# Optimization experiments

Measured on AMD Instinct MI355X. Metric: run time of the kernel, lower is better.

Reference implementation:

```python
import jax, jax.numpy as jnp
import numpy as np

N, E, F_IN, H, G, A, OUT = 50000, 800000, 128, 256, 64, 8, 1


def _lin(k, fi, fo):
    s = 1.0 / np.sqrt(fi)
    kw, kb = jax.random.split(k)
    W = jax.random.uniform(kw, (fi, fo), jnp.float32, -s, s)
    b = jax.random.uniform(kb, (fo,), jnp.float32, -s, s)
    return W, b


def setup_inputs() -> dict:
    key = jax.random.key(0)
    ks = jax.random.split(key, 12)
    x = jax.random.normal(ks[0], (N, F_IN), jnp.float32)
    edge_index = jax.random.randint(ks[1], (2, E), 0, N, dtype=jnp.int64)
    batch = jnp.sort(jax.random.randint(ks[2], (N,), 0, G, dtype=jnp.int64))
    graph_attr = jax.random.normal(ks[3], (G, A), jnp.float32)
    W1, b1 = _lin(ks[4], F_IN, H)
    W2, b2 = _lin(ks[5], H, H)
    W3, b3 = _lin(ks[6], H, H)
    fcW1, fcb1 = _lin(ks[7], H + A, H)
    fcW2, fcb2 = _lin(ks[8], H, OUT)
    ones = jnp.ones((H,), jnp.float32)
    zeros = jnp.zeros((H,), jnp.float32)
    return dict(x=x, graph_attr=graph_attr, edge_index=edge_index, batch=batch,
                W1=W1, b1=b1, W2=W2, b2=b2, W3=W3, b3=b3,
                g1=ones, be1=zeros, g2=ones, be2=zeros, g3=ones, be3=zeros,
                fcW1=fcW1, fcb1=fcb1, fcW2=fcW2, fcb2=fcb2)


def gcn_conv(x, W, b, src, dst, n):
    # PyG GCNConv: add self-loops, symmetric normalization, xW then scatter-add
    xw = x @ W  # [N, H]
    loop = jnp.arange(n)
    src2 = jnp.concatenate([src, loop])
    dst2 = jnp.concatenate([dst, loop])
    deg = jnp.zeros((n,), xw.dtype).at[dst2].add(1.0)
    dinv = jnp.where(deg > 0, jax.lax.rsqrt(deg), 0.0)
    norm = dinv[src2] * dinv[dst2]  # [E+N]
    out = jnp.zeros((n, xw.shape[1]), xw.dtype).at[dst2].add(xw[src2] * norm[:, None])
    return out + b


def layer_norm(x, g, b, eps=1e-5):
    m = x.mean(-1, keepdims=True)
    v = ((x - m) ** 2).mean(-1, keepdims=True)
    return (x - m) * jax.lax.rsqrt(v + eps) * g + b


def reference(x, graph_attr, edge_index, batch,
              W1, b1, W2, b2, W3, b3,
              g1, be1, g2, be2, g3, be3,
              fcW1, fcb1, fcW2, fcb2):
    src, dst = edge_index[0], edge_index[1]
    h = jax.nn.relu(layer_norm(gcn_conv(x, W1, b1, src, dst, N), g1, be1))
    h = jax.nn.relu(layer_norm(gcn_conv(h, W2, b2, src, dst, N), g2, be2))
    h = jax.nn.relu(layer_norm(gcn_conv(h, W3, b3, src, dst, N), g3, be3))
    # global mean pool over graph ids
    sums = jax.ops.segment_sum(h, batch, num_segments=G)
    cnts = jax.ops.segment_sum(jnp.ones((N,), h.dtype), batch, num_segments=G)
    pooled = sums / jnp.maximum(cnts, 1.0)[:, None]  # [G, H]
    z = jnp.concatenate([pooled, graph_attr.reshape(-1, A)], axis=1)
    z = jax.nn.relu(z @ fcW1 + fcb1)
    return z @ fcW2 + fcb2  # [G, OUT]
```

## Files before the change

### kernel.cpp

```cpp
#include <hip/hip_runtime.h>
#include <hip/hip_bf16.h>

#define N_NODES 50000
#define N_EDGES 800000
#define F_IN    128
#define H_DIM   256
#define G_NUM   64
#define A_DIM   8

#define NBUCKET 196
#define NCHUNK  391
#define CHUNK   2048
#define K4CAP   6144

typedef __attribute__((ext_vector_type(8))) short short8v;
typedef __attribute__((ext_vector_type(4))) float float4v;
typedef __attribute__((ext_vector_type(2))) float float2v;

__device__ __forceinline__ float b2f(unsigned short u) {
    return __uint_as_float(((unsigned int)u) << 16);
}
__device__ __forceinline__ unsigned short f2b(float v) {
    return __hip_bfloat16_raw(__float2bfloat16(v)).x;
}
__device__ __forceinline__ unsigned char f2fp8(float v) {
    return (unsigned char)(__builtin_amdgcn_cvt_pk_fp8_f32(v, v, 0, false) & 0xff);
}
__device__ __forceinline__ unsigned int pack2(float a, float b) {
    return (unsigned int)f2b(a) | ((unsigned int)f2b(b) << 16);
}
__device__ __forceinline__ void accadd16(float2v* a, uint4 v) {
    a[0] += __builtin_amdgcn_cvt_pk_f32_fp8((int)v.x, false);
    a[1] += __builtin_amdgcn_cvt_pk_f32_fp8((int)v.x, true);
    a[2] += __builtin_amdgcn_cvt_pk_f32_fp8((int)v.y, false);
    a[3] += __builtin_amdgcn_cvt_pk_f32_fp8((int)v.y, true);
    a[4] += __builtin_amdgcn_cvt_pk_f32_fp8((int)v.z, false);
    a[5] += __builtin_amdgcn_cvt_pk_f32_fp8((int)v.z, true);
    a[6] += __builtin_amdgcn_cvt_pk_f32_fp8((int)v.w, false);
    a[7] += __builtin_amdgcn_cvt_pk_f32_fp8((int)v.w, true);
}
__device__ __forceinline__ void accfma16(float2v* a, uint4 v, float w) {
    float2v w2 = {w, w};
    a[0] = __builtin_amdgcn_cvt_pk_f32_fp8((int)v.x, false) * w2 + a[0];
    a[1] = __builtin_amdgcn_cvt_pk_f32_fp8((int)v.x, true)  * w2 + a[1];
    a[2] = __builtin_amdgcn_cvt_pk_f32_fp8((int)v.y, false) * w2 + a[2];
    a[3] = __builtin_amdgcn_cvt_pk_f32_fp8((int)v.y, true)  * w2 + a[3];
    a[4] = __builtin_amdgcn_cvt_pk_f32_fp8((int)v.z, false) * w2 + a[4];
    a[5] = __builtin_amdgcn_cvt_pk_f32_fp8((int)v.z, true)  * w2 + a[5];
    a[6] = __builtin_amdgcn_cvt_pk_f32_fp8((int)v.w, false) * w2 + a[6];
    a[7] = __builtin_amdgcn_cvt_pk_f32_fp8((int)v.w, true)  * w2 + a[7];
}

#define SK 40


__global__ __launch_bounds__(512) void fuse0_kernel(const int* __restrict__ dst,
                                                    unsigned int* __restrict__ Hg,
                                                    const float* __restrict__ x,
                                                    const float* __restrict__ W1,
                                                    unsigned char* __restrict__ P8,
                                                    const float* __restrict__ W2,
                                                    unsigned short* __restrict__ Wt2,
                                                    const float* __restrict__ W3,
                                                    unsigned short* __restrict__ Wt3) {
    const int CB = NCHUNK;
    const int GB = (N_NODES + 127) / 128;
    int b = blockIdx.x, t = threadIdx.x;
    if (b < CB) {
        __shared__ unsigned int h[256];
        if (t < 256) h[t] = 0u;
        __syncthreads();
        int base = b * CHUNK;
        #pragma unroll
        for (int k = 0; k < 4; k++) {
            int i = base + k * 512 + t;
            if (i < N_EDGES) atomicAdd(&h[dst[i] >> 8], 1u);
        }
        __syncthreads();
        if (t < 256) Hg[(size_t)t * NCHUNK + b] = h[t];
        return;
    }
    b -= CB;
    if (b < GB) {
        __shared__ unsigned short As[128][SK];
        __shared__ unsigned short Bs[256][SK];
        int wave = t >> 6, lane = t & 63;
        int wm0 = (wave & 1) * 64, wn0 = (wave >> 1) * 64;
        int bm = b * 128;
        int l15 = lane & 15, lq = lane >> 4;
        float4v acc[4][4];
        #pragma unroll
        for (int i = 0; i < 4; i++)
            #pragma unroll
            for (int j = 0; j < 4; j++)
                acc[i][j] = (float4v){0.f, 0.f, 0.f, 0.f};

        for (int k0 = 0; k0 < F_IN; k0 += 32) {
            {
                int row = t >> 2, koff = (t & 3) * 8;
                short8v tmp = (short8v){0,0,0,0,0,0,0,0};
                if (bm + row < N_NODES) {
                    const float* xp = x + (size_t)(bm + row) * F_IN + k0 + koff;
                    float4 a0 = *(const float4*)xp;
                    float4 a1 = *(const float4*)(xp + 4);
                    tmp[0] = (short)f2b(a0.x); tmp[1] = (short)f2b(a0.y);
                    tmp[2] = (short)f2b(a0.z); tmp[3] = (short)f2b(a0.w);
                    tmp[4] = (short)f2b(a1.x); tmp[5] = (short)f2b(a1.y);
                    tmp[6] = (short)f2b(a1.z); tmp[7] = (short)f2b(a1.w);
                }
                *(short8v*)&As[row][koff] = tmp;
            }
            #pragma unroll
            for (int h = 0; h < 2; h++) {
                int c = t + h * 512;
                int n = c >> 2, koff = (c & 3) * 8;
                short8v tmp;
                #pragma unroll
                for (int kk = 0; kk < 8; kk++)
                    tmp[kk] = (short)f2b(W1[(size_t)(k0 + koff + kk) * H_DIM + n]);
                *(short8v*)&Bs[n][koff] = tmp;
            }
            __syncthreads();
            short8v af[4], bf[4];
            #pragma unroll
            for (int i = 0; i < 4; i++) {
                af[i] = *(const short8v*)&As[wm0 + i * 16 + l15][lq * 8];
                bf[i] = *(const short8v*)&Bs[wn0 + i * 16 + l15][lq * 8];
            }
            #pragma unroll
            for (int i = 0; i < 4; i++)
                #pragma unroll
                for (int j = 0; j < 4; j++)
                    acc[i][j] = __builtin_amdgcn_mfma_f32_16x16x32_bf16(af[i], bf[j], acc[i][j], 0, 0, 0);
            __syncthreads();
        }
        #pragma unroll
        for (int i = 0; i < 4; i++) {
            #pragma unroll
            for (int r = 0; r < 4; r++) {
                int row = bm + wm0 + i * 16 + lq * 4 + r;
                if (row < N_NODES) {
                    #pragma unroll
                    for (int j = 0; j < 4; j++) {
                        int col = wn0 + j * 16 + l15;
                        P8[(size_t)row * H_DIM + col] = f2fp8(acc[i][j][r]);
                    }
                }
            }
        }
        return;
    }
    b -= GB;
    int i = b * 512 + t;
    if (i < H_DIM * H_DIM) {
        int k = i >> 8, n = i & 255;
        Wt2[(size_t)n * H_DIM + k] = f2b(W2[i]);
    } else if (i < 2 * H_DIM * H_DIM) {
        int j = i - H_DIM * H_DIM;
        int k = j >> 8, n = j & 255;
        Wt3[(size_t)n * H_DIM + k] = f2b(W3[j]);
    }
}


__global__ __launch_bounds__(256) void scanH_kernel(unsigned int* __restrict__ Hg,
                                                    unsigned int* __restrict__ Btot) {
    __shared__ unsigned int tile[256];
    int b = blockIdx.x, t = threadIdx.x;
    unsigned int* row = Hg + (size_t)b * NCHUNK;
    int i0 = 2 * t, i1 = 2 * t + 1;
    unsigned int v0 = (i0 < NCHUNK) ? row[i0] : 0u;
    unsigned int v1 = (i1 < NCHUNK) ? row[i1] : 0u;
    unsigned int pair = v0 + v1;
    tile[t] = pair;
    __syncthreads();
    #pragma unroll
    for (int o = 1; o < 256; o <<= 1) {
        unsigned int add = (t >= o) ? tile[t - o] : 0u;
        __syncthreads();
        tile[t] += add;
        __syncthreads();
    }
    unsigned int excl = tile[t] - pair;
    if (i0 < NCHUNK) row[i0] = excl;
    if (i1 < NCHUNK) row[i1] = excl + v0;
    if (t == 255) Btot[b] = tile[255];
}

__global__ __launch_bounds__(256) void base_kernel(const unsigned int* __restrict__ Btot,
                                                   unsigned int* __restrict__ bucketBase,
                                                   const int* __restrict__ batch,
                                                   int* __restrict__ gstart,
                                                   int* __restrict__ rowptr,
                                                   float* __restrict__ pooled) {
    __shared__ unsigned int tile[256];
    int t = threadIdx.x;
    unsigned int v = (t < NBUCKET) ? Btot[t] : 0u;
    tile[t] = v;
    __syncthreads();
    #pragma unroll
    for (int o = 1; o < 256; o <<= 1) {
        unsigned int add = (t >= o) ? tile[t - o] : 0u;
        __syncthreads();
        tile[t] += add;
        __syncthreads();
    }
    if (t < NBUCKET) bucketBase[t] = tile[t] - v;
    if (t == NBUCKET - 1) bucketBase[NBUCKET] = tile[t];
    if (t == 0) rowptr[N_NODES] = N_EDGES;
    if (t <= G_NUM) {
        int lo = 0, hi = N_NODES;
        while (lo < hi) {
            int mid = (lo + hi) >> 1;
            if (batch[mid] < t) lo = mid + 1; else hi = mid;
        }
        gstart[t] = lo;
    }
    for (int i = t; i < G_NUM * H_DIM; i += 256) pooled[i] = 0.f;
}

__global__ __launch_bounds__(512) void scatter_kernel(const int* __restrict__ src,
                                                      const int* __restrict__ dst,
                                                      const unsigned int* __restrict__ Hg,
                                                      const unsigned int* __restrict__ bucketBase,
                                                      unsigned int* __restrict__ tmp) {
    __shared__ unsigned int off[256];
    int blk = blockIdx.x, t = threadIdx.x;
    if (t < 256)
        off[t] = (t < NBUCKET) ? (bucketBase[t] + Hg[(size_t)t * NCHUNK + blk]) : 0u;
    __syncthreads();
    int base = blk * CHUNK;
    #pragma unroll
    for (int k = 0; k < 4; k++) {
        int i = base + k * 512 + t;
        if (i < N_EDGES) {
            int d = dst[i], s = src[i];
            unsigned int slot = atomicAdd(&off[d >> 8], 1u);
            tmp[slot] = ((unsigned int)(d & 255) << 16) | (unsigned int)s;
        }
    }
}

__global__ __launch_bounds__(256) void finalize_kernel(const unsigned int* __restrict__ tmp,
                                                       const unsigned int* __restrict__ bucketBase,
                                                       int* __restrict__ rowptr,
                                                       float* __restrict__ dinv,
                                                       unsigned short* __restrict__ csr_src) {
    __shared__ unsigned int te[K4CAP];
    __shared__ unsigned int h2[256];
    __shared__ unsigned int sc[256];
    __shared__ unsigned int off2[256];
    int b = blockIdx.x, t = threadIdx.x;
    unsigned int beg = bucketBase[b], end = bucketBase[b + 1];
    int cnt = (int)(end - beg);
    bool lds_ok = (cnt <= K4CAP);
    h2[t] = 0u;
    __syncthreads();
    for (int i = t; i < cnt; i += 256) {
        unsigned int u = tmp[beg + i];
        if (lds_ok) te[i] = u;
        atomicAdd(&h2[u >> 16], 1u);
    }
    __syncthreads();
    unsigned int c = h2[t];
    sc[t] = c;
    __syncthreads();
    #pragma unroll
    for (int o = 1; o < 256; o <<= 1) {
        unsigned int add = (t >= o) ? sc[t - o] : 0u;
        __syncthreads();
        sc[t] += add;
        __syncthreads();
    }
    unsigned int excl = sc[t] - c;
    int v = (b << 8) + t;
    if (v < N_NODES) {
        rowptr[v] = (int)(beg + excl);
        dinv[v] = rsqrtf((float)c + 1.0f);
    }
    off2[t] = excl;
    __syncthreads();
    for (int i = t; i < cnt; i += 256) {
        unsigned int u = lds_ok ? te[i] : tmp[beg + i];
        unsigned int lo = u >> 16;
        unsigned int s2 = atomicAdd(&off2[lo], 1u);
        csr_src[beg + s2] = (unsigned short)(u & 0xFFFFu);
    }
}


__global__ __launch_bounds__(512) void gemm_f8(const unsigned short* __restrict__ A,
                                               const unsigned short* __restrict__ Bt,
                                               unsigned char* __restrict__ C8,
                                               const float* __restrict__ dinv,
                                               int M, int K) {
    __shared__ unsigned short As[128][SK];
    __shared__ unsigned short Bs[256][SK];
    int t = threadIdx.x;
    int wave = t >> 6, lane = t & 63;
    int wm0 = (wave & 1) * 64, wn0 = (wave >> 1) * 64;
    int bm = blockIdx.x * 128;
    int l15 = lane & 15, lq = lane >> 4;
    float4v acc[4][4];
    #pragma unroll
    for (int i = 0; i < 4; i++)
        #pragma unroll
        for (int j = 0; j < 4; j++)
            acc[i][j] = (float4v){0.f, 0.f, 0.f, 0.f};

    for (int k0 = 0; k0 < K; k0 += 32) {
        {
            int row = t >> 2, koff = (t & 3) * 8;
            uint4 va = make_uint4(0u, 0u, 0u, 0u);
            if (bm + row < M)
                va = *(const uint4*)(A + (size_t)(bm + row) * K + k0 + koff);
            *(uint4*)&As[row][koff] = va;
        }
        #pragma unroll
        for (int h = 0; h < 2; h++) {
            int c = t + h * 512;
            int row = c >> 2, koff = (c & 3) * 8;
            uint4 vb = *(const uint4*)(Bt + (size_t)row * K + k0 + koff);
            *(uint4*)&Bs[row][koff] = vb;
        }
        __syncthreads();
        short8v af[4], bf[4];
        #pragma unroll
        for (int i = 0; i < 4; i++) {
            af[i] = *(const short8v*)&As[wm0 + i * 16 + l15][lq * 8];
            bf[i] = *(const short8v*)&Bs[wn0 + i * 16 + l15][lq * 8];
        }
        #pragma unroll
        for (int i = 0; i < 4; i++)
            #pragma unroll
            for (int j = 0; j < 4; j++)
                acc[i][j] = __builtin_amdgcn_mfma_f32_16x16x32_bf16(af[i], bf[j], acc[i][j], 0, 0, 0);
        __syncthreads();
    }
    #pragma unroll
    for (int i = 0; i < 4; i++) {
        #pragma unroll
        for (int r = 0; r < 4; r++) {
            int row = bm + wm0 + i * 16 + lq * 4 + r;
            if (row < M) {
                float dv = dinv[row];
                #pragma unroll
                for (int j = 0; j < 4; j++) {
                    int col = wn0 + j * 16 + l15;
                    C8[(size_t)row * H_DIM + col] = f2fp8(dv * acc[i][j][r]);
                }
            }
        }
    }
}


template<int F, bool DO_LN, bool W8>
__global__ __launch_bounds__(256) void gather_ns(const unsigned char* __restrict__ xw,
                                                 unsigned short* __restrict__ out,
                                                 const int* __restrict__ rowptr,
                                                 const unsigned short* __restrict__ csr_src,
                                                 const float* __restrict__ dinv,
                                                 const float* __restrict__ bias,
                                                 const float* __restrict__ gamma,
                                                 const float* __restrict__ beta) {
    constexpr int BPL = F / 16;
    constexpr int NF2 = BPL / 2;
    int lane = threadIdx.x & 63;
    int wave = threadIdx.x >> 6;
    int p = lane & 15;
    int gbase = lane & 48;
    int node = blockIdx.x * 16 + wave * 4 + (lane >> 4);
    int beg = rowptr[node];
    int deg = rowptr[node + 1] - beg;
    float d = dinv[node];
    const unsigned char* xp = xw + (size_t)p * BPL;

    float2v acc2[NF2];
    #pragma unroll
    for (int k = 0; k < NF2; k++) acc2[k] = (float2v){0.f, 0.f};

    {
        uint4 v = *(const uint4*)(xp + (size_t)node * F);
        if constexpr (W8) accfma16(acc2, v, d);
        else              accadd16(acc2, v);
    }

    int sv = 0; float wv = 0.f;
    if (p < deg) {
        sv = (int)csr_src[beg + p];
        if constexpr (W8) wv = dinv[sv];
    }

    for (int b0 = 0; b0 < deg; b0 += 16) {
        int m = deg - b0; if (m > 16) m = 16;
        int sv_n = 0; float wv_n = 0.f;
        int rem = deg - b0 - 16;
        if (rem > 0 && p < rem) {
            sv_n = (int)csr_src[beg + b0 + 16 + p];
            if constexpr (W8) wv_n = dinv[sv_n];
        }
        int j = 0;
        for (; j + 8 <= m; j += 8) {
            int s0 = __shfl(sv, gbase | j, 64);
            int s1 = __shfl(sv, gbase | (j + 1), 64);
            int s2 = __shfl(sv, gbase | (j + 2), 64);
            int s3 = __shfl(sv, gbase | (j + 3), 64);
            int s4 = __shfl(sv, gbase | (j + 4), 64);
            int s5 = __shfl(sv, gbase | (j + 5), 64);
            int s6 = __shfl(sv, gbase | (j + 6), 64);
            int s7 = __shfl(sv, gbase | (j + 7), 64);
            uint4 v0 = *(const uint4*)(xp + (size_t)s0 * F);
            uint4 v1 = *(const uint4*)(xp + (size_t)s1 * F);
            uint4 v2 = *(const uint4*)(xp + (size_t)s2 * F);
            uint4 v3 = *(const uint4*)(xp + (size_t)s3 * F);
            uint4 v4 = *(const uint4*)(xp + (size_t)s4 * F);
            uint4 v5 = *(const uint4*)(xp + (size_t)s5 * F);
            uint4 v6 = *(const uint4*)(xp + (size_t)s6 * F);
            uint4 v7 = *(const uint4*)(xp + (size_t)s7 * F);
            if constexpr (W8) {
                float w0 = __shfl(wv, gbase | j, 64);
                float w1 = __shfl(wv, gbase | (j + 1), 64);
                float w2 = __shfl(wv, gbase | (j + 2), 64);
                float w3 = __shfl(wv, gbase | (j + 3), 64);
                float w4 = __shfl(wv, gbase | (j + 4), 64);
                float w5 = __shfl(wv, gbase | (j + 5), 64);
                float w6 = __shfl(wv, gbase | (j + 6), 64);
                float w7 = __shfl(wv, gbase | (j + 7), 64);
                accfma16(acc2, v0, w0); accfma16(acc2, v1, w1);
                accfma16(acc2, v2, w2); accfma16(acc2, v3, w3);
                accfma16(acc2, v4, w4); accfma16(acc2, v5, w5);
                accfma16(acc2, v6, w6); accfma16(acc2, v7, w7);
            } else {
                accadd16(acc2, v0); accadd16(acc2, v1);
                accadd16(acc2, v2); accadd16(acc2, v3);
                accadd16(acc2, v4); accadd16(acc2, v5);
                accadd16(acc2, v6); accadd16(acc2, v7);
            }
        }
        for (; j + 4 <= m; j += 4) {
            int s0 = __shfl(sv, gbase | j, 64);
            int s1 = __shfl(sv, gbase | (j + 1), 64);
            int s2 = __shfl(sv, gbase | (j + 2), 64);
            int s3 = __shfl(sv, gbase | (j + 3), 64);
            uint4 v0 = *(const uint4*)(xp + (size_t)s0 * F);
            uint4 v1 = *(const uint4*)(xp + (size_t)s1 * F);
            uint4 v2 = *(const uint4*)(xp + (size_t)s2 * F);
            uint4 v3 = *(const uint4*)(xp + (size_t)s3 * F);
            if constexpr (W8) {
                float w0 = __shfl(wv, gbase | j, 64);
                float w1 = __shfl(wv, gbase | (j + 1), 64);
                float w2 = __shfl(wv, gbase | (j + 2), 64);
                float w3 = __shfl(wv, gbase | (j + 3), 64);
                accfma16(acc2, v0, w0); accfma16(acc2, v1, w1);
                accfma16(acc2, v2, w2); accfma16(acc2, v3, w3);
            } else {
                accadd16(acc2, v0); accadd16(acc2, v1);
                accadd16(acc2, v2); accadd16(acc2, v3);
            }
        }
        for (; j < m; ++j) {
            int s0 = __shfl(sv, gbase | j, 64);
            uint4 v0 = *(const uint4*)(xp + (size_t)s0 * F);
            if constexpr (W8) {
                float w0 = __shfl(wv, gbase | j, 64);
                accfma16(acc2, v0, w0);
            } else {
                accadd16(acc2, v0);
            }
        }
        sv = sv_n; wv = wv_n;
    }

    float v[BPL];
    #pragma unroll
    for (int k = 0; k < NF2; k++) { v[2 * k] = d * acc2[k].x; v[2 * k + 1] = d * acc2[k].y; }

    if constexpr (DO_LN) {
        #pragma unroll
        for (int q = 0; q < BPL / 4; q++) {
            float4 bi = ((const float4*)bias)[p * (BPL / 4) + q];
            v[q * 4 + 0] += bi.x; v[q * 4 + 1] += bi.y;
            v[q * 4 + 2] += bi.z; v[q * 4 + 3] += bi.w;
        }
        float s = 0.f, ss = 0.f;
        #pragma unroll
        for (int k = 0; k < BPL; k++) { s += v[k]; ss += v[k] * v[k]; }
        #pragma unroll
        for (int o = 1; o < 16; o <<= 1) {
            s  += __shfl_xor(s, o, 64);
            ss += __shfl_xor(ss, o, 64);
        }
        float mn = s * (1.f / F);
        float var = ss * (1.f / F) - mn * mn;
        float rstd = rsqrtf(var + 1e-5f);
        #pragma unroll
        for (int q = 0; q < BPL / 4; q++) {
            float4 ga = ((const float4*)gamma)[p * (BPL / 4) + q];
            float4 be = ((const float4*)beta)[p * (BPL / 4) + q];
            v[q * 4 + 0] = fmaxf((v[q * 4 + 0] - mn) * rstd * ga.x + be.x, 0.f);
            v[q * 4 + 1] = fmaxf((v[q * 4 + 1] - mn) * rstd * ga.y + be.y, 0.f);
            v[q * 4 + 2] = fmaxf((v[q * 4 + 2] - mn) * rstd * ga.z + be.z, 0.f);
            v[q * 4 + 3] = fmaxf((v[q * 4 + 3] - mn) * rstd * ga.w + be.w, 0.f);
        }
    }

    unsigned short* op = out + (size_t)node * F + p * BPL;
    uint4 o0;
    o0.x = pack2(v[0], v[1]); o0.y = pack2(v[2], v[3]);
    o0.z = pack2(v[4], v[5]); o0.w = pack2(v[6], v[7]);
    *(uint4*)op = o0;
    if constexpr (F == 256) {
        uint4 o1;
        o1.x = pack2(v[8],  v[9]);  o1.y = pack2(v[10], v[11]);
        o1.z = pack2(v[12], v[13]); o1.w = pack2(v[14], v[15]);
        *(uint4*)(op + 8) = o1;
    }
}


__global__ __launch_bounds__(128) void pool_kernel(const unsigned int* __restrict__ h32,
                                                   const int* __restrict__ batch,
                                                   float* __restrict__ pooled, int n) {
    int t = threadIdx.x;
    int start = blockIdx.x * 64;
    int end = min(start + 64, n);
    if (start >= n) return;
    int cur = batch[start];
    float a0 = 0.f, a1 = 0.f;
    for (int i = start; i < end; ++i) {
        int g = batch[i];
        if (g != cur) {
            atomicAdd(&pooled[(size_t)cur * H_DIM + 2 * t], a0);
            atomicAdd(&pooled[(size_t)cur * H_DIM + 2 * t + 1], a1);
            a0 = a1 = 0.f;
            cur = g;
        }
        unsigned int u = h32[(size_t)i * (H_DIM / 2) + t];
        a0 += b2f((unsigned short)(u & 0xffffu));
        a1 += b2f((unsigned short)(u >> 16));
    }
    atomicAdd(&pooled[(size_t)cur * H_DIM + 2 * t], a0);
    atomicAdd(&pooled[(size_t)cur * H_DIM + 2 * t + 1], a1);
}


__global__ __launch_bounds__(256) void fc_kernel(const float* __restrict__ pooled,
                                                 const int* __restrict__ gstart,
                                                 const float* __restrict__ gattr,
                                                 const float* __restrict__ fcW1,
                                                 const float* __restrict__ fcb1,
                                                 const float* __restrict__ fcW2,
                                                 const float* __restrict__ fcb2,
                                                 float* __restrict__ out) {
    __shared__ float zc[H_DIM + A_DIM];
    __shared__ float z1[H_DIM];
    int g = blockIdx.x, t = threadIdx.x;
    int c_i = gstart[g + 1] - gstart[g];
    float c = (float)(c_i > 1 ? c_i : 1);
    zc[t] = pooled[(size_t)g * H_DIM + t] / c;
    if (t < A_DIM) zc[H_DIM + t] = gattr[g * A_DIM + t];
    __syncthreads();
    float s = fcb1[t];
    for (int k = 0; k < H_DIM + A_DIM; k++)
        s += zc[k] * fcW1[(size_t)k * H_DIM + t];
    z1[t] = fmaxf(s, 0.f) * fcW2[t];
    __syncthreads();
    for (int off = 128; off; off >>= 1) {
        if (t < off) z1[t] += z1[t + off];
        __syncthreads();
    }
    if (t == 0) out[g] = z1[0] + fcb2[0];
}


extern "C" void kernel_launch(void* const* d_in, const int* in_sizes, int n_in,
                              void* d_out, int out_size, void* d_ws, size_t ws_size,
                              hipStream_t stream) {
    const float* x     = (const float*)d_in[0];
    const float* gattr = (const float*)d_in[1];
    const int*   ei    = (const int*)d_in[2];
    const int*   batch = (const int*)d_in[3];
    const float* W1 = (const float*)d_in[4];  const float* b1 = (const float*)d_in[5];
    const float* W2 = (const float*)d_in[6];  const float* b2 = (const float*)d_in[7];
    const float* W3 = (const float*)d_in[8];  const float* b3 = (const float*)d_in[9];
    const float* g1 = (const float*)d_in[10]; const float* be1 = (const float*)d_in[11];
    const float* g2 = (const float*)d_in[12]; const float* be2 = (const float*)d_in[13];
    const float* g3 = (const float*)d_in[14]; const float* be3 = (const float*)d_in[15];
    const float* fcW1 = (const float*)d_in[16]; const float* fcb1 = (const float*)d_in[17];
    const float* fcW2 = (const float*)d_in[18]; const float* fcb2 = (const float*)d_in[19];
    float* out = (float*)d_out;

    char* w = (char*)d_ws;
    unsigned char*  Pb8 = (unsigned char*)w;  w += (size_t)N_NODES * H_DIM;
    unsigned short* Hb  = (unsigned short*)w; w += (size_t)N_NODES * H_DIM * 2;
    unsigned short* Wt2 = (unsigned short*)w; w += (size_t)H_DIM * H_DIM * 2;
    unsigned short* Wt3 = (unsigned short*)w; w += (size_t)H_DIM * H_DIM * 2;
    float* dinv   = (float*)w; w += (size_t)N_NODES * 4;
    float* pooled = (float*)w; w += (size_t)G_NUM * H_DIM * 4;
    int* rowptr   = (int*)w;   w += (size_t)(N_NODES + 4) * 4;
    unsigned int* Hg = (unsigned int*)w;      w += (size_t)256 * NCHUNK * 4;
    unsigned int* Btot = (unsigned int*)w;    w += (size_t)256 * 4;
    unsigned int* bucketBase = (unsigned int*)w; w += (size_t)(NBUCKET + 4) * 4;
    unsigned int* tmp = (unsigned int*)w;     w += (size_t)N_EDGES * 4;
    unsigned short* csr_src = (unsigned short*)w; w += (size_t)N_EDGES * 2;
    int* gstart   = (int*)w;   w += (size_t)(G_NUM + 1) * 4;

    const int* srcp = ei;
    const int* dstp = ei + N_EDGES;

    {
        const int CB = NCHUNK;
        const int GB = (N_NODES + 127) / 128;
        const int WB = (2 * H_DIM * H_DIM + 511) / 512;
        fuse0_kernel<<<CB + GB + WB, 512, 0, stream>>>(dstp, Hg, x, W1, Pb8, W2, Wt2, W3, Wt3);
    }
    scanH_kernel<<<NBUCKET, 256, 0, stream>>>(Hg, Btot);
    base_kernel<<<1, 256, 0, stream>>>(Btot, bucketBase, batch, gstart, rowptr, pooled);
    scatter_kernel<<<NCHUNK, 512, 0, stream>>>(srcp, dstp, Hg, bucketBase, tmp);
    finalize_kernel<<<NBUCKET, 256, 0, stream>>>(tmp, bucketBase, rowptr, dinv, csr_src);

    int gemm_blocks = (N_NODES + 127) / 128;
    int gather_blocks = N_NODES / 16;

    gather_ns<H_DIM, true, true><<<gather_blocks, 256, 0, stream>>>(Pb8, Hb, rowptr, csr_src,
                                                                    dinv, b1, g1, be1);
    gemm_f8<<<gemm_blocks, 512, 0, stream>>>(Hb, Wt2, Pb8, dinv, N_NODES, H_DIM);
    gather_ns<H_DIM, true, false><<<gather_blocks, 256, 0, stream>>>(Pb8, Hb, rowptr, csr_src,
                                                                     dinv, b2, g2, be2);
    gemm_f8<<<gemm_blocks, 512, 0, stream>>>(Hb, Wt3, Pb8, dinv, N_NODES, H_DIM);
    gather_ns<H_DIM, true, false><<<gather_blocks, 256, 0, stream>>>(Pb8, Hb, rowptr, csr_src,
                                                                     dinv, b3, g3, be3);

    pool_kernel<<<(N_NODES + 63) / 64, 128, 0, stream>>>((const unsigned int*)Hb, batch, pooled, N_NODES);
    fc_kernel<<<G_NUM, 256, 0, stream>>>(pooled, gstart, gattr, fcW1, fcb1, fcW2, fcb2, out);
}
```

Measured before the change: 336.6 us.

## Overlap GCN gather and FP8 GEMM via quarter-split fused launches

Merges the gather/LayerNorm kernel and the FP8 GEMM into one launch that dispatches blocks by index. Each layer is split into four node quarters, so the GEMM on quarter q-1 runs in the same launch as the gather on quarter q. A second FP8 buffer is added so the GEMM output and the gather input alternate between layers. The aim is to overlap the memory-latency-bound gather with the compute-bound GEMM. In exchange there are more launches, and gather blocks carry the GEMM's shared-memory allocation, which may lower their occupancy.

```diff
diff --git a/kernel.cpp b/kernel.cpp
--- a/kernel.cpp
+++ b/kernel.cpp
@@ -12,6 +12,7 @@
 #define NCHUNK  391
 #define CHUNK   2048
 #define K4CAP   6144
+#define QN      12500
 
 typedef __attribute__((ext_vector_type(8))) short short8v;
 typedef __attribute__((ext_vector_type(4))) float float4v;
@@ -289,17 +290,16 @@
 }
 
 
-__global__ __launch_bounds__(512) void gemm_f8(const unsigned short* __restrict__ A,
-                                               const unsigned short* __restrict__ Bt,
-                                               unsigned char* __restrict__ C8,
-                                               const float* __restrict__ dinv,
-                                               int M, int K) {
+__device__ __forceinline__ void gemm_body_f8(const unsigned short* __restrict__ A,
+                                             const unsigned short* __restrict__ Bt,
+                                             unsigned char* __restrict__ C8,
+                                             const float* __restrict__ dinv,
+                                             int M, int K, int bm) {
     __shared__ unsigned short As[128][SK];
     __shared__ unsigned short Bs[256][SK];
     int t = threadIdx.x;
     int wave = t >> 6, lane = t & 63;
     int wm0 = (wave & 1) * 64, wn0 = (wave >> 1) * 64;
-    int bm = blockIdx.x * 128;
     int l15 = lane & 15, lq = lane >> 4;
     float4v acc[4][4];
     #pragma unroll
@@ -355,33 +355,27 @@
 }
 
 
-template<int F, bool DO_LN, bool W8>
-__global__ __launch_bounds__(256) void gather_ns(const unsigned char* __restrict__ xw,
-                                                 unsigned short* __restrict__ out,
-                                                 const int* __restrict__ rowptr,
-                                                 const unsigned short* __restrict__ csr_src,
-                                                 const float* __restrict__ dinv,
-                                                 const float* __restrict__ bias,
-                                                 const float* __restrict__ gamma,
-                                                 const float* __restrict__ beta) {
-    constexpr int BPL = F / 16;
-    constexpr int NF2 = BPL / 2;
-    int lane = threadIdx.x & 63;
-    int wave = threadIdx.x >> 6;
-    int p = lane & 15;
-    int gbase = lane & 48;
-    int node = blockIdx.x * 16 + wave * 4 + (lane >> 4);
+template<bool W8>
+__device__ __forceinline__ void gather_body(const unsigned char* __restrict__ xw,
+                                            unsigned short* __restrict__ out,
+                                            const int* __restrict__ rowptr,
+                                            const unsigned short* __restrict__ csr_src,
+                                            const float* __restrict__ dinv,
+                                            const float* __restrict__ bias,
+                                            const float* __restrict__ gamma,
+                                            const float* __restrict__ beta,
+                                            int node, int p, int gbase) {
     int beg = rowptr[node];
     int deg = rowptr[node + 1] - beg;
     float d = dinv[node];
-    const unsigned char* xp = xw + (size_t)p * BPL;
-
-    float2v acc2[NF2];
-    #pragma unroll
-    for (int k = 0; k < NF2; k++) acc2[k] = (float2v){0.f, 0.f};
+    const unsigned char* xp = xw + (size_t)p * 16;
+
+    float2v acc2[8];
+    #pragma unroll
+    for (int k = 0; k < 8; k++) acc2[k] = (float2v){0.f, 0.f};
 
     {
-        uint4 v = *(const uint4*)(xp + (size_t)node * F);
+        uint4 v = *(const uint4*)(xp + (size_t)node * H_DIM);
         if constexpr (W8) accfma16(acc2, v, d);
         else              accadd16(acc2, v);
     }
@@ -410,14 +404,14 @@
             int s5 = __shfl(sv, gbase | (j + 5), 64);
             int s6 = __shfl(sv, gbase | (j + 6), 64);
             int s7 = __shfl(sv, gbase | (j + 7), 64);
-            uint4 v0 = *(const uint4*)(xp + (size_t)s0 * F);
-            uint4 v1 = *(const uint4*)(xp + (size_t)s1 * F);
-            uint4 v2 = *(const uint4*)(xp + (size_t)s2 * F);
-            uint4 v3 = *(const uint4*)(xp + (size_t)s3 * F);
-            uint4 v4 = *(const uint4*)(xp + (size_t)s4 * F);
-            uint4 v5 = *(const uint4*)(xp + (size_t)s5 * F);
-            uint4 v6 = *(const uint4*)(xp + (size_t)s6 * F);
-            uint4 v7 = *(const uint4*)(xp + (size_t)s7 * F);
+            uint4 v0 = *(const uint4*)(xp + (size_t)s0 * H_DIM);
+            uint4 v1 = *(const uint4*)(xp + (size_t)s1 * H_DIM);
+            uint4 v2 = *(const uint4*)(xp + (size_t)s2 * H_DIM);
+            uint4 v3 = *(const uint4*)(xp + (size_t)s3 * H_DIM);
+            uint4 v4 = *(const uint4*)(xp + (size_t)s4 * H_DIM);
+            uint4 v5 = *(const uint4*)(xp + (size_t)s5 * H_DIM);
+            uint4 v6 = *(const uint4*)(xp + (size_t)s6 * H_DIM);
+            uint4 v7 = *(const uint4*)(xp + (size_t)s7 * H_DIM);
             if constexpr (W8) {
                 float w0 = __shfl(wv, gbase | j, 64);
                 float w1 = __shfl(wv, gbase | (j + 1), 64);
@@ -443,10 +437,10 @@
             int s1 = __shfl(sv, gbase | (j + 1), 64);
             int s2 = __shfl(sv, gbase | (j + 2), 64);
             int s3 = __shfl(sv, gbase | (j + 3), 64);
-            uint4 v0 = *(const uint4*)(xp + (size_t)s0 * F);
-            uint4 v1 = *(const uint4*)(xp + (size_t)s1 * F);
-            uint4 v2 = *(const uint4*)(xp + (size_t)s2 * F);
-            uint4 v3 = *(const uint4*)(xp + (size_t)s3 * F);
+            uint4 v0 = *(const uint4*)(xp + (size_t)s0 * H_DIM);
+            uint4 v1 = *(const uint4*)(xp + (size_t)s1 * H_DIM);
+            uint4 v2 = *(const uint4*)(xp + (size_t)s2 * H_DIM);
+            uint4 v3 = *(const uint4*)(xp + (size_t)s3 * H_DIM);
             if constexpr (W8) {
                 float w0 = __shfl(wv, gbase | j, 64);
                 float w1 = __shfl(wv, gbase | (j + 1), 64);
@@ -461,7 +455,7 @@
         }
         for (; j < m; ++j) {
             int s0 = __shfl(sv, gbase | j, 64);
-            uint4 v0 = *(const uint4*)(xp + (size_t)s0 * F);
+            uint4 v0 = *(const uint4*)(xp + (size_t)s0 * H_DIM);
             if constexpr (W8) {
                 float w0 = __shfl(wv, gbase | j, 64);
                 accfma16(acc2, v0, w0);
@@ -472,50 +466,71 @@
         sv = sv_n; wv = wv_n;
     }
 
-    float v[BPL];
-    #pragma unroll
-    for (int k = 0; k < NF2; k++) { v[2 * k] = d * acc2[k].x; v[2 * k + 1] = d * acc2[k].y; }
-
-    if constexpr (DO_LN) {
-        #pragma unroll
-        for (int q = 0; q < BPL / 4; q++) {
-            float4 bi = ((const float4*)bias)[p * (BPL / 4) + q];
-            v[q * 4 + 0] += bi.x; v[q * 4 + 1] += bi.y;
-            v[q * 4 + 2] += bi.z; v[q * 4 + 3] += bi.w;
-        }
-        float s = 0.f, ss = 0.f;
-        #pragma unroll
-        for (int k = 0; k < BPL; k++) { s += v[k]; ss += v[k] * v[k]; }
-        #pragma unroll
-        for (int o = 1; o < 16; o <<= 1) {
-            s  += __shfl_xor(s, o, 64);
-            ss += __shfl_xor(ss, o, 64);
-        }
-        float mn = s * (1.f / F);
-        float var = ss * (1.f / F) - mn * mn;
-        float rstd = rsqrtf(var + 1e-5f);
-        #pragma unroll
-        for (int q = 0; q < BPL / 4; q++) {
-            float4 ga = ((const float4*)gamma)[p * (BPL / 4) + q];
-            float4 be = ((const float4*)beta)[p * (BPL / 4) + q];
-            v[q * 4 + 0] = fmaxf((v[q * 4 + 0] - mn) * rstd * ga.x + be.x, 0.f);
-            v[q * 4 + 1] = fmaxf((v[q * 4 + 1] - mn) * rstd * ga.y + be.y, 0.f);
-            v[q * 4 + 2] = fmaxf((v[q * 4 + 2] - mn) * rstd * ga.z + be.z, 0.f);
-            v[q * 4 + 3] = fmaxf((v[q * 4 + 3] - mn) * rstd * ga.w + be.w, 0.f);
-        }
-    }
-
-    unsigned short* op = out + (size_t)node * F + p * BPL;
-    uint4 o0;
-    o0.x = pack2(v[0], v[1]); o0.y = pack2(v[2], v[3]);
-    o0.z = pack2(v[4], v[5]); o0.w = pack2(v[6], v[7]);
+    float v[16];
+    #pragma unroll
+    for (int k = 0; k < 8; k++) { v[2 * k] = d * acc2[k].x; v[2 * k + 1] = d * acc2[k].y; }
+
+    #pragma unroll
+    for (int q = 0; q < 4; q++) {
+        float4 bi = ((const float4*)bias)[p * 4 + q];
+        v[q * 4 + 0] += bi.x; v[q * 4 + 1] += bi.y;
+        v[q * 4 + 2] += bi.z; v[q * 4 + 3] += bi.w;
+    }
+    float s = 0.f, ss = 0.f;
+    #pragma unroll
+    for (int k = 0; k < 16; k++) { s += v[k]; ss += v[k] * v[k]; }
+    #pragma unroll
+    for (int o = 1; o < 16; o <<= 1) {
+        s  += __shfl_xor(s, o, 64);
+        ss += __shfl_xor(ss, o, 64);
+    }
+    float mn = s * (1.f / H_DIM);
+    float var = ss * (1.f / H_DIM) - mn * mn;
+    float rstd = rsqrtf(var + 1e-5f);
+    #pragma unroll
+    for (int q = 0; q < 4; q++) {
+        float4 ga = ((const float4*)gamma)[p * 4 + q];
+        float4 be = ((const float4*)beta)[p * 4 + q];
+        v[q * 4 + 0] = fmaxf((v[q * 4 + 0] - mn) * rstd * ga.x + be.x, 0.f);
+        v[q * 4 + 1] = fmaxf((v[q * 4 + 1] - mn) * rstd * ga.y + be.y, 0.f);
+        v[q * 4 + 2] = fmaxf((v[q * 4 + 2] - mn) * rstd * ga.z + be.z, 0.f);
+        v[q * 4 + 3] = fmaxf((v[q * 4 + 3] - mn) * rstd * ga.w + be.w, 0.f);
+    }
+
+    unsigned short* op = out + (size_t)node * H_DIM + p * 16;
+    uint4 o0, o1;
+    o0.x = pack2(v[0], v[1]);   o0.y = pack2(v[2], v[3]);
+    o0.z = pack2(v[4], v[5]);   o0.w = pack2(v[6], v[7]);
+    o1.x = pack2(v[8], v[9]);   o1.y = pack2(v[10], v[11]);
+    o1.z = pack2(v[12], v[13]); o1.w = pack2(v[14], v[15]);
     *(uint4*)op = o0;
-    if constexpr (F == 256) {
-        uint4 o1;
-        o1.x = pack2(v[8],  v[9]);  o1.y = pack2(v[10], v[11]);
-        o1.z = pack2(v[12], v[13]); o1.w = pack2(v[14], v[15]);
-        *(uint4*)(op + 8) = o1;
-    }
+    *(uint4*)(op + 8) = o1;
+}
+
+
+template<bool W8>
+__global__ __launch_bounds__(512) void gg_kernel(int GBk, int nstart, int nend,
+                                                 const unsigned char* __restrict__ Pin,
+                                                 unsigned short* __restrict__ Hb,
+                                                 int mstart, int mend,
+                                                 const unsigned short* __restrict__ Wt,
+                                                 unsigned char* __restrict__ Pout,
+                                                 const int* __restrict__ rowptr,
+                                                 const unsigned short* __restrict__ csr_src,
+                                                 const float* __restrict__ dinv,
+                                                 const float* __restrict__ bias,
+                                                 const float* __restrict__ gamma,
+                                                 const float* __restrict__ beta) {
+    int b = blockIdx.x;
+    if (b < GBk) {
+        int lane = threadIdx.x & 63, wave = threadIdx.x >> 6;
+        int node = nstart + b * 32 + wave * 4 + (lane >> 4);
+        if (node >= nend) return;
+        gather_body<W8>(Pin, Hb, rowptr, csr_src, dinv, bias, gamma, beta,
+                        node, lane & 15, lane & 48);
+        return;
+    }
+    gemm_body_f8(Hb, Wt, Pout, dinv, mend, H_DIM, mstart + (b - GBk) * 128);
 }
 
 
@@ -592,8 +607,9 @@
     float* out = (float*)d_out;
 
     char* w = (char*)d_ws;
-    unsigned char*  Pb8 = (unsigned char*)w;  w += (size_t)N_NODES * H_DIM;
-    unsigned short* Hb  = (unsigned short*)w; w += (size_t)N_NODES * H_DIM * 2;
+    unsigned char*  Pb8  = (unsigned char*)w; w += (size_t)N_NODES * H_DIM;
+    unsigned char*  Pb8b = (unsigned char*)w; w += (size_t)N_NODES * H_DIM;
+    unsigned short* Hb   = (unsigned short*)w; w += (size_t)N_NODES * H_DIM * 2;
     unsigned short* Wt2 = (unsigned short*)w; w += (size_t)H_DIM * H_DIM * 2;
     unsigned short* Wt3 = (unsigned short*)w; w += (size_t)H_DIM * H_DIM * 2;
     float* dinv   = (float*)w; w += (size_t)N_NODES * 4;
@@ -620,18 +636,31 @@
     scatter_kernel<<<NCHUNK, 512, 0, stream>>>(srcp, dstp, Hg, bucketBase, tmp);
     finalize_kernel<<<NBUCKET, 256, 0, stream>>>(tmp, bucketBase, rowptr, dinv, csr_src);
 
-    int gemm_blocks = (N_NODES + 127) / 128;
-    int gather_blocks = N_NODES / 16;
-
-    gather_ns<H_DIM, true, true><<<gather_blocks, 256, 0, stream>>>(Pb8, Hb, rowptr, csr_src,
-                                                                    dinv, b1, g1, be1);
-    gemm_f8<<<gemm_blocks, 512, 0, stream>>>(Hb, Wt2, Pb8, dinv, N_NODES, H_DIM);
-    gather_ns<H_DIM, true, false><<<gather_blocks, 256, 0, stream>>>(Pb8, Hb, rowptr, csr_src,
-                                                                     dinv, b2, g2, be2);
-    gemm_f8<<<gemm_blocks, 512, 0, stream>>>(Hb, Wt3, Pb8, dinv, N_NODES, H_DIM);
-    gather_ns<H_DIM, true, false><<<gather_blocks, 256, 0, stream>>>(Pb8, Hb, rowptr, csr_src,
-                                                                     dinv, b3, g3, be3);
-
+    const int GQB = (QN + 31) / 32;
+    const int MQB = (QN + 127) / 128;
+
+    for (int q = 0; q < 5; ++q) {
+        int GBk = (q < 4) ? GQB : 0;
+        int MBk = (q > 0) ? MQB : 0;
+        int ns = q * QN, ms = (q - 1) * QN;
+        gg_kernel<true><<<GBk + MBk, 512, 0, stream>>>(GBk, ns, ns + QN, Pb8, Hb,
+                                                       ms, ms + QN, Wt2, Pb8b,
+                                                       rowptr, csr_src, dinv, b1, g1, be1);
+    }
+    for (int q = 0; q < 5; ++q) {
+        int GBk = (q < 4) ? GQB : 0;
+        int MBk = (q > 0) ? MQB : 0;
+        int ns = q * QN, ms = (q - 1) * QN;
+        gg_kernel<false><<<GBk + MBk, 512, 0, stream>>>(GBk, ns, ns + QN, Pb8b, Hb,
+                                                        ms, ms + QN, Wt3, Pb8,
+                                                        rowptr, csr_src, dinv, b2, g2, be2);
+    }
+    {
+        const int GBk = (N_NODES + 31) / 32;
+        gg_kernel<false><<<GBk, 512, 0, stream>>>(GBk, 0, N_NODES, Pb8, Hb,
+                                                  0, 0, Wt3, Pb8b,
+                                                  rowptr, csr_src, dinv, b3, g3, be3);
+    }
     pool_kernel<<<(N_NODES + 63) / 64, 128, 0, stream>>>((const unsigned int*)Hb, batch, pooled, N_NODES);
     fc_kernel<<<G_NUM, 256, 0, stream>>>(pooled, gstart, gattr, fcW1, fcb1, fcW2, fcb2, out);
 }
```

New measurement: 400.2 us. 18.9% more time.
